# Optimization experiments

Measured on AMD Instinct MI355X. Metric: run time of the kernel, lower is better.

The kernel has to match this reference:

```python
import jax, jax.numpy as jnp
import numpy as np

EMBED_DIM = 1024
NUM_HEADS = 16
NUM_GLOBAL = 4
NUM_LOCAL = NUM_HEADS - NUM_GLOBAL
WINDOW = 256
HEAD_DIM = EMBED_DIM // NUM_HEADS


def setup_inputs() -> dict:
    key = jax.random.key(0)
    k1, k2, k3 = jax.random.split(key, 3)
    B, S = 4, 2048
    x = jax.random.normal(k1, (B, S, EMBED_DIM), dtype=jnp.float32)
    w_qkv = jax.random.normal(k2, (EMBED_DIM, 3 * EMBED_DIM), dtype=jnp.float32) * (EMBED_DIM ** -0.5)
    b_qkv = jnp.zeros((3 * EMBED_DIM,), dtype=jnp.float32)
    w_out = jax.random.normal(k3, (EMBED_DIM, EMBED_DIM), dtype=jnp.float32) * (EMBED_DIM ** -0.5)
    b_out = jnp.zeros((EMBED_DIM,), dtype=jnp.float32)
    return {"x": x, "w_qkv": w_qkv, "b_qkv": b_qkv, "w_out": w_out, "b_out": b_out}


def _masks(seq_len):
    i = jnp.arange(seq_len)[:, None]
    j = jnp.arange(seq_len)[None, :]
    diff = i - j
    global_mask = diff < 0                      # True = masked (strictly future)
    local_mask = (diff < 0) | (diff > WINDOW)   # True = masked (outside window)
    return global_mask, local_mask


def _attend(q, k, v, mask):
    # q,k,v: [B,h,S,D]; mask: [S,S] True = disallow
    scores = jnp.einsum('bhqd,bhkd->bhqk', q, k) * (HEAD_DIM ** -0.5)
    scores = jnp.where(mask[None, None], -jnp.inf, scores)
    w = jax.nn.softmax(scores, axis=-1)
    return jnp.einsum('bhqk,bhkd->bhqd', w, v)


def reference(x, w_qkv, b_qkv, w_out, b_out):
    B, S, _ = x.shape
    qkv = x @ w_qkv + b_qkv                      # [B,S,3E]
    q, k, v = jnp.split(qkv, 3, axis=-1)
    def heads(t):
        return t.reshape(B, S, NUM_HEADS, HEAD_DIM).transpose(0, 2, 1, 3)
    q, k, v = heads(q), heads(k), heads(v)       # [B,H,S,D]
    gmask, lmask = _masks(S)
    ctx_g = _attend(q[:, :NUM_GLOBAL], k[:, :NUM_GLOBAL], v[:, :NUM_GLOBAL], gmask)
    ctx_l = _attend(q[:, NUM_GLOBAL:], k[:, NUM_GLOBAL:], v[:, NUM_GLOBAL:], lmask)
    ctx = jnp.concatenate([ctx_g, ctx_l], axis=1)          # [B,H,S,D]
    ctx = ctx.transpose(0, 2, 1, 3).reshape(B, S, EMBED_DIM)
    return ctx @ w_out + b_out
```

## Files before the change

### kernel.cpp

```cpp
#include <hip/hip_runtime.h>
#include <stdint.h>

#define EMB 1024
#define SEQ 2048
#define NB 4
#define NH 16
#define HD 64
#define NGLOB 4
#define WIN 256
#define MTOT (NB*SEQ)
#define NQKV (3*EMB)

typedef __attribute__((ext_vector_type(8))) short bf16x8;
typedef __attribute__((ext_vector_type(4))) float f32x4;
typedef __attribute__((ext_vector_type(16))) float f32x16;
typedef unsigned short u16;
typedef unsigned int u32;

__device__ __forceinline__ u16 f2bf(float f) {
  u32 u = __builtin_bit_cast(u32, f);
  u += 0x7fffu + ((u >> 16) & 1u);
  return (u16)(u >> 16);
}

__device__ __forceinline__ u32 pack2bf(float a, float b) {
  return (u32)f2bf(a) | ((u32)f2bf(b) << 16);
}

#define MFMA16(a, b, c) __builtin_amdgcn_mfma_f32_16x16x32_bf16(a, b, c, 0, 0, 0)
#define MFMA32(a, b, c) __builtin_amdgcn_mfma_f32_32x32x16_bf16(a, b, c, 0, 0, 0)
#define GLD16(g, l) __builtin_amdgcn_global_load_lds( \
    (const __attribute__((address_space(1))) void*)(g), \
    (__attribute__((address_space(3))) void*)(l), 16, 0, 0)

__global__ void k_cast(const float* __restrict__ in, u16* __restrict__ out, int n4) {
  int i = blockIdx.x * blockDim.x + threadIdx.x;
  if (i >= n4) return;
  float4 f = ((const float4*)in)[i];
  ushort4 o;
  o.x = f2bf(f.x); o.y = f2bf(f.y); o.z = f2bf(f.z); o.w = f2bf(f.w);
  ((ushort4*)out)[i] = o;
}

__global__ void k_transpose_cast(const float* __restrict__ w, u16* __restrict__ wt,
                                 int R, int C) {
  __shared__ float tile[32][33];
  int c0 = blockIdx.x * 32, r0 = blockIdx.y * 32;
  int tx = threadIdx.x, ty = threadIdx.y;
  #pragma unroll
  for (int j = 0; j < 32; j += 8)
    tile[ty + j][tx] = w[(size_t)(r0 + ty + j) * C + (c0 + tx)];
  __syncthreads();
  #pragma unroll
  for (int j = 0; j < 32; j += 8)
    wt[(size_t)(c0 + ty + j) * R + (r0 + tx)] = f2bf(tile[tx][ty + j]);
}

template <int EPI>
__global__ __launch_bounds__(256, 2) void k_gemm(
    const u16* __restrict__ A, const u16* __restrict__ Bt,
    const float* __restrict__ bias,
    u16* __restrict__ Qo, u16* __restrict__ Ko, u16* __restrict__ Vt,
    float* __restrict__ outp) {
  __shared__ __align__(16) u16 ldsA[128 * 64];
  __shared__ __align__(16) u16 ldsB[128 * 64];
  const int tid = threadIdx.x;
  const int w = tid >> 6, lane = tid & 63;
  const int wm = w >> 1, wn = w & 1;
  const int m0 = blockIdx.x * 128, n0 = blockIdx.y * 128;
  const int rq = lane & 15, g = lane >> 4;

  const int srow = lane >> 3;
  const int scol = ((lane & 7) ^ srow) << 3;

  f32x4 acc[4][4] = {};
  char* ldsAb = (char*)ldsA;
  char* ldsBb = (char*)ldsB;

  for (int k0 = 0; k0 < EMB; k0 += 64) {
    #pragma unroll
    for (int it = 0; it < 4; ++it) {
      int t = w * 4 + it;
      int row = t * 8 + srow;
      GLD16(A + (size_t)(m0 + row) * EMB + k0 + scol, ldsAb + t * 1024);
      GLD16(Bt + (size_t)(n0 + row) * EMB + k0 + scol, ldsBb + t * 1024);
    }
    __syncthreads();
    #pragma unroll
    for (int ks = 0; ks < 2; ++ks) {
      bf16x8 af[4], bfr[4];
      #pragma unroll
      for (int i = 0; i < 4; ++i) {
        int rowA = wm * 64 + i * 16 + rq;
        int off = (ks * 64 + (g << 4)) ^ ((rowA & 7) << 4);
        af[i] = *(const bf16x8*)(ldsAb + rowA * 128 + off);
        int rowB = wn * 64 + i * 16 + rq;
        int offb = (ks * 64 + (g << 4)) ^ ((rowB & 7) << 4);
        bfr[i] = *(const bf16x8*)(ldsBb + rowB * 128 + offb);
      }
      #pragma unroll
      for (int mi = 0; mi < 4; ++mi)
        #pragma unroll
        for (int ni = 0; ni < 4; ++ni)
          acc[mi][ni] = MFMA16(af[mi], bfr[ni], acc[mi][ni]);
    }
    __syncthreads();
  }

  #pragma unroll
  for (int ni = 0; ni < 4; ++ni) {
    int col = n0 + wn * 64 + ni * 16 + rq;
    float bv = bias[col];
    if (EPI == 0) {
      int part = col >> 10;
      int hh = (col & 1023) >> 6;
      int d = col & 63;
      #pragma unroll
      for (int mi = 0; mi < 4; ++mi) {
        #pragma unroll
        for (int i = 0; i < 4; ++i) {
          int m = m0 + wm * 64 + mi * 16 + g * 4 + i;
          int b = m >> 11, s = m & 2047;
          u16 val = f2bf(acc[mi][ni][i] + bv);
          size_t bh = (size_t)(b * NH + hh);
          if (part == 0)      Qo[(bh * SEQ + s) * HD + d] = val;
          else if (part == 1) Ko[(bh * SEQ + s) * HD + d] = val;
          else                Vt[(bh * HD + d) * SEQ + s] = val;
        }
      }
    } else {
      #pragma unroll
      for (int mi = 0; mi < 4; ++mi)
        #pragma unroll
        for (int i = 0; i < 4; ++i) {
          int m = m0 + wm * 64 + mi * 16 + g * 4 + i;
          outp[(size_t)m * EMB + col] = acc[mi][ni][i] + bv;
        }
    }
  }
}

__global__ __launch_bounds__(256, 4) void k_attn(
    const u16* __restrict__ Q, const u16* __restrict__ K,
    const u16* __restrict__ Vt, u16* __restrict__ ctx) {
  const int w = threadIdx.x >> 6, lane = threadIdx.x & 63;
  const int l31 = lane & 31;
  const int hi = lane >> 5;
  const bool hib = hi != 0;
  const int hi8 = hi * 8, hi4 = hi * 4;

  const int gid = blockIdx.x;
  const int type = gid >> 8;
  const int k = gid & 255;
  int bh, qt;
  if (type < 2) {
    int pk = type * 256 + k;
    int bg = pk & 15;
    int q0 = pk >> 4;
    int sel = (w + k) & 3;
    if (sel < 2) {
      bh = (bg >> 2) * 16 + (bg & 3);
      qt = sel == 0 ? q0 : 63 - q0;
    } else {
      int lidx = pk * 2 + (sel - 2);
      int bl = lidx >> 6;
      bh = (bl / 12) * 16 + 4 + (bl % 12);
      qt = lidx & 63;
    }
  } else {
    int bk = (type - 2) * 256 + k;
    int lidx = 1024 + bk * 4 + w;
    int bl = lidx >> 6;
    bh = (bl / 12) * 16 + 4 + (bl % 12);
    qt = lidx & 63;
  }

  const int qb = qt * 32;
  const int h = bh & 15;
  const int b = bh >> 4;
  const bool isloc = (h >= NGLOB);

  const u16* Qp = Q + (size_t)bh * SEQ * HD;
  const u16* Kp = K + (size_t)bh * SEQ * HD;
  const u16* Vp = Vt + (size_t)bh * HD * SEQ;

  const int q = qb + l31;

  bf16x8 qf[4];
  #pragma unroll
  for (int j = 0; j < 4; ++j)
    qf[j] = *(const bf16x8*)(Qp + (size_t)q * HD + j * 16 + hi8);

  f32x16 oacc[2] = {};
  float m = -__builtin_inff();
  float l = 0.f;

  int klo = 0;
  if (isloc && qb > WIN) klo = qb - WIN;

  for (int kc = klo; kc <= qb; kc += 32) {
    f32x16 s = {};
    #pragma unroll
    for (int j = 0; j < 4; ++j) {
      bf16x8 kf = *(const bf16x8*)(Kp + (size_t)(kc + l31) * HD + j * 16 + hi8);
      s = MFMA32(kf, qf[j], s);
    }

    float p[16];
    float cmax = -__builtin_inff();
    #pragma unroll
    for (int r = 0; r < 16; ++r) {
      int key = kc + hi4 + (r & 3) + 8 * (r >> 2);
      float v = s[r] * 0.125f;
      bool msk = (key > q) || (isloc && (q - key > WIN));
      p[r] = msk ? -__builtin_inff() : v;
      cmax = fmaxf(cmax, p[r]);
    }
    cmax = fmaxf(cmax, __shfl_xor(cmax, 32));

    float mu;
    if (__any(cmax > m + 8.f)) {
      float mn = fmaxf(m, cmax);
      mu = (mn == -__builtin_inff()) ? 0.f : mn;
      float f = __expf(((m == -__builtin_inff()) ? mu : m) - mu);
      m = mn;
      l *= f;
      #pragma unroll
      for (int dt = 0; dt < 2; ++dt)
        #pragma unroll
        for (int r = 0; r < 16; ++r)
          oacc[dt][r] *= f;
    } else {
      mu = (m == -__builtin_inff()) ? 0.f : m;
    }

    float psum = 0.f;
    #pragma unroll
    for (int r = 0; r < 16; ++r) {
      p[r] = __expf(p[r] - mu);
      psum += p[r];
    }
    psum += __shfl_xor(psum, 32);
    l += psum;

    union { u32 u[4]; bf16x8 v; } pbf[2];
    #pragma unroll
    for (int sl = 0; sl < 2; ++sl) {
      int s8 = sl * 8;
      u32 X0 = pack2bf(p[s8 + 0], p[s8 + 1]);
      u32 X1 = pack2bf(p[s8 + 2], p[s8 + 3]);
      u32 X2 = pack2bf(p[s8 + 4], p[s8 + 5]);
      u32 X3 = pack2bf(p[s8 + 6], p[s8 + 7]);
      u32 oX0 = (u32)__shfl_xor((int)X0, 32);
      u32 oX1 = (u32)__shfl_xor((int)X1, 32);
      u32 oX2 = (u32)__shfl_xor((int)X2, 32);
      u32 oX3 = (u32)__shfl_xor((int)X3, 32);
      pbf[sl].u[0] = hib ? oX2 : X0;
      pbf[sl].u[1] = hib ? oX3 : X1;
      pbf[sl].u[2] = hib ? X2 : oX0;
      pbf[sl].u[3] = hib ? X3 : oX1;
    }

    #pragma unroll
    for (int dt = 0; dt < 2; ++dt) {
      #pragma unroll
      for (int sl = 0; sl < 2; ++sl) {
        bf16x8 vf = *(const bf16x8*)(Vp + (size_t)(dt * 32 + l31) * SEQ + kc + sl * 16 + hi8);
        oacc[dt] = MFMA32(vf, pbf[sl].v, oacc[dt]);
      }
    }
  }

  float linv = 1.f / l;
  #pragma unroll
  for (int dt = 0; dt < 2; ++dt) {
    #pragma unroll
    for (int r = 0; r < 16; ++r) {
      int d = dt * 32 + hi4 + (r & 3) + 8 * (r >> 2);
      int e = h * HD + d;
      ctx[(size_t)(b * SEQ + q) * EMB + e] = f2bf(oacc[dt][r] * linv);
    }
  }
}

extern "C" void kernel_launch(void* const* d_in, const int* in_sizes, int n_in,
                              void* d_out, int out_size, void* d_ws, size_t ws_size,
                              hipStream_t stream) {
  const float* x     = (const float*)d_in[0];
  const float* w_qkv = (const float*)d_in[1];
  const float* b_qkv = (const float*)d_in[2];
  const float* w_out = (const float*)d_in[3];
  const float* b_out = (const float*)d_in[4];
  float* out = (float*)d_out;

  char* ws = (char*)d_ws;
  u16* xb    = (u16*)(ws);
  u16* wqkvT = (u16*)(ws + (16ull << 20));
  u16* woutT = (u16*)(ws + (22ull << 20));
  u16* Qb    = (u16*)(ws + (24ull << 20));
  u16* Kb    = (u16*)(ws + (40ull << 20));
  u16* Vt    = (u16*)(ws + (56ull << 20));
  u16* ctx   = (u16*)(ws + (72ull << 20));

  k_cast<<<(MTOT * EMB / 4) / 256, 256, 0, stream>>>(x, xb, MTOT * EMB / 4);
  dim3 tb(32, 8);
  k_transpose_cast<<<dim3(NQKV / 32, EMB / 32), tb, 0, stream>>>(w_qkv, wqkvT, EMB, NQKV);
  k_transpose_cast<<<dim3(EMB / 32, EMB / 32), tb, 0, stream>>>(w_out, woutT, EMB, EMB);

  k_gemm<0><<<dim3(MTOT / 128, NQKV / 128), 256, 0, stream>>>(
      xb, wqkvT, b_qkv, Qb, Kb, Vt, nullptr);

  k_attn<<<dim3(NB * NH * (SEQ / 128)), 256, 0, stream>>>(Qb, Kb, Vt, ctx);

  k_gemm<1><<<dim3(MTOT / 128, EMB / 128), 256, 0, stream>>>(
      ctx, woutT, b_out, nullptr, nullptr, nullptr, out);
}
```

Before: 212.1 us.

## Split global-head attention key range across warps with LSE merge in LDS

Global (causal full) heads now give each 32-query tile a whole block, splitting the key chunks across the four warps (split-K flash attention) and merging partial outputs through shared memory with a log-sum-exp combine. Local heads keep one warp per tile. The aim is to remove the long tail from global-head tiles with many key chunks and balance work better; the grid grows and launch bounds rise to 7 waves. The cost is a __syncthreads, LDS traffic, bf16 rounding of the partial outputs before the merge, and possible register-pressure spills under the tighter launch bound.

After: 558.7 us. 2.63x slower.

```diff
diff --git a/kernel.cpp b/kernel.cpp
--- a/kernel.cpp
+++ b/kernel.cpp
@@ -21,6 +21,11 @@
   u32 u = __builtin_bit_cast(u32, f);
   u += 0x7fffu + ((u >> 16) & 1u);
   return (u16)(u >> 16);
+}
+
+__device__ __forceinline__ float bf2f(u16 v) {
+  u32 u = (u32)v << 16;
+  return __builtin_bit_cast(float, u);
 }
 
 __device__ __forceinline__ u32 pack2bf(float a, float b) {
@@ -140,9 +145,12 @@
   }
 }
 
-__global__ __launch_bounds__(256, 4) void k_attn(
+__global__ __launch_bounds__(256, 7) void k_attn(
     const u16* __restrict__ Q, const u16* __restrict__ K,
     const u16* __restrict__ Vt, u16* __restrict__ ctx) {
+  __shared__ u16 Obuf[4][64][36];
+  __shared__ float m_s[4][32], l_s[4][32];
+
   const int w = threadIdx.x >> 6, lane = threadIdx.x & 63;
   const int l31 = lane & 31;
   const int hi = lane >> 5;
@@ -150,35 +158,33 @@
   const int hi8 = hi * 8, hi4 = hi * 4;
 
   const int gid = blockIdx.x;
-  const int type = gid >> 8;
-  const int k = gid & 255;
-  int bh, qt;
-  if (type < 2) {
-    int pk = type * 256 + k;
-    int bg = pk & 15;
-    int q0 = pk >> 4;
-    int sel = (w + k) & 3;
-    if (sel < 2) {
-      bh = (bg >> 2) * 16 + (bg & 3);
-      qt = sel == 0 ? q0 : 63 - q0;
-    } else {
-      int lidx = pk * 2 + (sel - 2);
-      int bl = lidx >> 6;
-      bh = (bl / 12) * 16 + 4 + (bl % 12);
-      qt = lidx & 63;
-    }
+  const bool isglob = gid < 1024;
+
+  int bh, qt, cstart, clen;
+  if (isglob) {
+    int bg = gid & 15;
+    int j = gid >> 4;
+    qt = ((j & 3) << 4) | (j >> 2);
+    bh = (bg >> 2) * 16 + (bg & 3);
+    int L = qt + 1;
+    int base = L >> 2, rem = L & 3;
+    clen = base + (w < rem ? 1 : 0);
+    cstart = w * base + (w < rem ? w : rem);
   } else {
-    int bk = (type - 2) * 256 + k;
-    int lidx = 1024 + bk * 4 + w;
+    int lidx = (gid - 1024) * 4 + w;
     int bl = lidx >> 6;
     bh = (bl / 12) * 16 + 4 + (bl % 12);
     qt = lidx & 63;
+    int qb_ = qt * 32;
+    int klo = (qb_ > WIN) ? qb_ - WIN : 0;
+    cstart = klo >> 5;
+    clen = qt + 1 - cstart;
   }
 
   const int qb = qt * 32;
   const int h = bh & 15;
   const int b = bh >> 4;
-  const bool isloc = (h >= NGLOB);
+  const bool isloc = !isglob;
 
   const u16* Qp = Q + (size_t)bh * SEQ * HD;
   const u16* Kp = K + (size_t)bh * SEQ * HD;
@@ -195,10 +201,8 @@
   float m = -__builtin_inff();
   float l = 0.f;
 
-  int klo = 0;
-  if (isloc && qb > WIN) klo = qb - WIN;
-
-  for (int kc = klo; kc <= qb; kc += 32) {
+  int kc = cstart * 32;
+  for (int it = 0; it < clen; ++it, kc += 32) {
     f32x16 s = {};
     #pragma unroll
     for (int j = 0; j < 4; ++j) {
@@ -271,14 +275,43 @@
     }
   }
 
-  float linv = 1.f / l;
-  #pragma unroll
-  for (int dt = 0; dt < 2; ++dt) {
-    #pragma unroll
-    for (int r = 0; r < 16; ++r) {
-      int d = dt * 32 + hi4 + (r & 3) + 8 * (r >> 2);
-      int e = h * HD + d;
-      ctx[(size_t)(b * SEQ + q) * EMB + e] = f2bf(oacc[dt][r] * linv);
+  if (isglob) {
+    if (hi == 0) { m_s[w][l31] = m; l_s[w][l31] = l; }
+    #pragma unroll
+    for (int dt = 0; dt < 2; ++dt)
+      #pragma unroll
+      for (int r = 0; r < 16; ++r) {
+        int d = dt * 32 + hi4 + (r & 3) + 8 * (r >> 2);
+        Obuf[w][d][l31] = f2bf(oacc[dt][r]);
+      }
+    __syncthreads();
+
+    const int tid = threadIdx.x;
+    const int dd = tid & 63;
+    const int qg = tid >> 6;
+    #pragma unroll
+    for (int i = 0; i < 8; ++i) {
+      int qq = qg * 8 + i;
+      float m0v = m_s[0][qq], m1v = m_s[1][qq], m2v = m_s[2][qq], m3v = m_s[3][qq];
+      float M = fmaxf(fmaxf(m0v, m1v), fmaxf(m2v, m3v));
+      float w0 = __expf(m0v - M), w1 = __expf(m1v - M);
+      float w2 = __expf(m2v - M), w3 = __expf(m3v - M);
+      float L = w0 * l_s[0][qq] + w1 * l_s[1][qq] + w2 * l_s[2][qq] + w3 * l_s[3][qq];
+      float val = w0 * bf2f(Obuf[0][dd][qq]) + w1 * bf2f(Obuf[1][dd][qq]) +
+                  w2 * bf2f(Obuf[2][dd][qq]) + w3 * bf2f(Obuf[3][dd][qq]);
+      int s = qb + qq;
+      ctx[(size_t)(b * SEQ + s) * EMB + h * HD + dd] = f2bf(val / L);
+    }
+  } else {
+    float linv = 1.f / l;
+    #pragma unroll
+    for (int dt = 0; dt < 2; ++dt) {
+      #pragma unroll
+      for (int r = 0; r < 16; ++r) {
+        int d = dt * 32 + hi4 + (r & 3) + 8 * (r >> 2);
+        int e = h * HD + d;
+        ctx[(size_t)(b * SEQ + q) * EMB + e] = f2bf(oacc[dt][r] * linv);
+      }
     }
   }
 }
@@ -310,7 +343,7 @@
   k_gemm<0><<<dim3(MTOT / 128, NQKV / 128), 256, 0, stream>>>(
       xb, wqkvT, b_qkv, Qb, Kb, Vt, nullptr);
 
-  k_attn<<<dim3(NB * NH * (SEQ / 128)), 256, 0, stream>>>(Qb, Kb, Vt, ctx);
+  k_attn<<<dim3(1024 + 768), 256, 0, stream>>>(Qb, Kb, Vt, ctx);
 
   k_gemm<1><<<dim3(MTOT / 128, EMB / 128), 256, 0, stream>>>(
       ctx, woutT, b_out, nullptr, nullptr, nullptr, out);
```
